# Performance work log

Hardware: AMD Instinct MI355X
Metric: run time of the kernel (lower is better)

## Reference

```python
import jax, jax.numpy as jnp
import numpy as np

TEMPERATURE = 0.02
B, T, D = 32, 256, 128


def _l2norm(x):
    return x / jnp.linalg.norm(x, axis=-1, keepdims=True)


def setup_inputs() -> dict:
    key = jax.random.key(0)
    k1, k2, k3, k4, k5, k6 = jax.random.split(key, 6)
    query_single = _l2norm(jax.random.normal(k1, (B, D), dtype=jnp.float32))
    pos_single = _l2norm(jax.random.normal(k2, (B, D), dtype=jnp.float32))
    query_multi = _l2norm(jax.random.normal(k3, (B, T, D), dtype=jnp.float32))
    pos_multi = _l2norm(jax.random.normal(k4, (B, T, D), dtype=jnp.float32))
    # variable-length masks (at least 1 valid token each, like real tokenized batches)
    q_len = jax.random.randint(k5, (B,), T // 4, T + 1)
    p_len = jax.random.randint(k6, (B,), T // 4, T + 1)
    pos = jnp.arange(T)[None, :]
    q_mask = pos < q_len[:, None]
    p_mask = pos < p_len[:, None]
    return {
        "query_single": query_single,
        "pos_single": pos_single,
        "query_multi": query_multi,
        "pos_multi": pos_multi,
        "q_mask": q_mask,
        "p_mask": p_mask,
    }


def _late_interaction_similarity(q_tokens, q_mask, p_tokens, p_mask):
    # All-pairs token similarity: [Bq, Bp, Tq, Tp]
    sim = jnp.einsum("bqd,cpd->bcqp", q_tokens, p_tokens)
    neg = jnp.finfo(sim.dtype).min
    sim = jnp.where(p_mask[None, :, None, :], sim, neg)
    mx = jnp.max(sim, axis=-1)                       # [Bq, Bp, Tq]
    mx = jnp.where(q_mask[:, None, :], mx, 0.0)      # drop invalid query tokens
    s = jnp.sum(mx, axis=-1)                         # [Bq, Bp]
    t_i = jnp.maximum(jnp.sum(q_mask, axis=-1), 1).astype(sim.dtype)  # [Bq]
    return s / t_i[:, None]


def _diag_cross_entropy(logits):
    # labels = arange(B): standard in-batch InfoNCE
    logp = jax.nn.log_softmax(logits, axis=-1)
    return -jnp.mean(jnp.diagonal(logp))


def reference(query_single, pos_single, query_multi, pos_multi, q_mask, p_mask):
    tau = TEMPERATURE
    dense_sim = query_single @ pos_single.T                       # [B, B]
    single_loss = _diag_cross_entropy(dense_sim / tau)

    S_late = _late_interaction_similarity(query_multi, q_mask, pos_multi, p_mask)
    multi_loss = _diag_cross_entropy(S_late / tau)

    dense_probs = jax.nn.softmax(dense_sim / tau, axis=1)
    late_probs = jax.nn.softmax(S_late / tau, axis=1)
    eps = 1e-8
    kl = jnp.mean(jnp.sum(dense_probs * jnp.log((dense_probs + eps) / (late_probs + eps)), axis=1))

    total_loss = single_loss + multi_loss + kl
    return (total_loss, single_loss, multi_loss, kl)
```

## Files before the change

### kernel.cpp

```cpp
#include <hip/hip_runtime.h>
#include <hip/hip_bf16.h>

#define B_SZ 32
#define T_SZ 256
#define D_SZ 128
#define TAU_INV 50.0f

typedef __bf16 bf16x8 __attribute__((ext_vector_type(8)));
typedef float f32x4 __attribute__((ext_vector_type(4)));

__device__ __forceinline__ unsigned short f2bf(float f) {
    union { float f; unsigned int u; } v; v.f = f;
    unsigned int r = v.u + 0x7fffu + ((v.u >> 16) & 1u);
    return (unsigned short)(r >> 16);
}

__device__ __forceinline__ bool mask_is_byte(const void* m) {
    return ((const int*)m)[0] != 1;
}
__device__ __forceinline__ int mget(const void* m, int idx, bool isb) {
    return isb ? (((const unsigned char*)m)[idx] != 0) : (((const int*)m)[idx] != 0);
}

__global__ __launch_bounds__(256) void cvt_both(
    const float* __restrict__ qsrc, const float* __restrict__ psrc,
    unsigned short* __restrict__ Qb, unsigned short* __restrict__ Pb) {
    const int half = blockIdx.x >> 10;
    const float* s = half ? psrc : qsrc;
    unsigned short* d = half ? Pb : Qb;
    int i = ((blockIdx.x & 1023) * 256 + threadIdx.x) * 4;
    float4 v = *(const float4*)(s + i);
    ushort4 o;
    o.x = f2bf(v.x); o.y = f2bf(v.y); o.z = f2bf(v.z); o.w = f2bf(v.w);
    *(ushort4*)(d + i) = o;
}

__global__ __launch_bounds__(512, 4) void late_sim(
    const unsigned short* __restrict__ Qbf, const unsigned short* __restrict__ Pbf,
    const void* __restrict__ qmask, const void* __restrict__ pmask,
    float* __restrict__ sraw)
{
    __shared__ __align__(16) unsigned char Plds[T_SZ * D_SZ * 2];
    __shared__ float madd[T_SZ];
    __shared__ float qmul[2][T_SZ];
    __shared__ float wsum[2][8];

    const int tid = threadIdx.x;
    const int l   = tid & 63;
    const int w   = tid >> 6;
    const int bid = blockIdx.x;
    const int c   = bid & 31;
    const int bg  = bid >> 5;
    const int b0  = bg, b1 = bg + 16;
    const int lr  = l & 15;
    const int lg  = l >> 4;

    const bool isb = mask_is_byte(qmask);
    const unsigned short* Pc = Pbf + c * (T_SZ * D_SZ);

    int p_hi;
    {
        int v = 0;
        #pragma unroll
        for (int j = 0; j < 4; ++j)
            if (mget(pmask, c * T_SZ + l * 4 + j, isb)) v = l * 4 + j + 1;
        #pragma unroll
        for (int off = 1; off < 64; off <<= 1) {
            int o = __shfl_xor(v, off);
            v = v > o ? v : o;
        }
        p_hi = v > 1 ? v : 1;
    }
    const int ptmax   = (p_hi + 15) >> 4;
    const int stiters = (p_hi + 31) >> 5;

    const int qrow = w * 32 + (l & 31);
    const bool do0 = __any(mget(qmask, b0 * T_SZ + qrow, isb));
    const bool do1 = __any(mget(qmask, b1 * T_SZ + qrow, isb));

    for (int it = 0; it < stiters; ++it) {
        int m   = it * 512 + tid;
        int row = m >> 4;
        int cs  = m & 15;
        bf16x8 v = *(const bf16x8*)(Pc + m * 8);
        *(bf16x8*)(Plds + row * 256 + ((cs ^ (row & 7)) << 4)) = v;
    }
    {
        int t = tid & 255;
        if (tid < 256) madd[t] = mget(pmask, c * T_SZ + t, isb) ? 0.0f : -1e30f;
        qmul[tid >> 8][t] = mget(qmask, (tid < 256 ? b0 : b1) * T_SZ + t, isb) ? 1.0f : 0.0f;
    }

    bf16x8 qf0[2][4] = {}, qf1[2][4] = {};
    if (do0)
        #pragma unroll
        for (int qt = 0; qt < 2; ++qt)
            #pragma unroll
            for (int k = 0; k < 4; ++k)
                qf0[qt][k] = *(const bf16x8*)(Qbf + b0 * (T_SZ * D_SZ)
                                              + (w * 32 + qt * 16 + lr) * D_SZ + k * 32 + lg * 8);
    if (do1)
        #pragma unroll
        for (int qt = 0; qt < 2; ++qt)
            #pragma unroll
            for (int k = 0; k < 4; ++k)
                qf1[qt][k] = *(const bf16x8*)(Qbf + b1 * (T_SZ * D_SZ)
                                              + (w * 32 + qt * 16 + lr) * D_SZ + k * 32 + lg * 8);

    __syncthreads();

    float r00 = -3e38f, r01 = -3e38f, r10 = -3e38f, r11 = -3e38f;

    for (int pt = 0; pt < ptmax; ++pt) {
        f32x4 a00 = {0,0,0,0}, a01 = {0,0,0,0}, a10 = {0,0,0,0}, a11 = {0,0,0,0};
        #pragma unroll
        for (int k = 0; k < 4; ++k) {
            int row = pt * 16 + lr;
            bf16x8 af = *(const bf16x8*)(Plds + row * 256 + (((k * 4 + lg) ^ (row & 7)) << 4));
            if (do0) {
                a00 = __builtin_amdgcn_mfma_f32_16x16x32_bf16(af, qf0[0][k], a00, 0, 0, 0);
                a01 = __builtin_amdgcn_mfma_f32_16x16x32_bf16(af, qf0[1][k], a01, 0, 0, 0);
            }
            if (do1) {
                a10 = __builtin_amdgcn_mfma_f32_16x16x32_bf16(af, qf1[0][k], a10, 0, 0, 0);
                a11 = __builtin_amdgcn_mfma_f32_16x16x32_bf16(af, qf1[1][k], a11, 0, 0, 0);
            }
        }
        float pm0 = madd[pt * 16 + lg * 4 + 0];
        float pm1 = madd[pt * 16 + lg * 4 + 1];
        float pm2 = madd[pt * 16 + lg * 4 + 2];
        float pm3 = madd[pt * 16 + lg * 4 + 3];
        if (do0) {
            r00 = fmaxf(r00, fmaxf(fmaxf(a00[0]+pm0, a00[1]+pm1), fmaxf(a00[2]+pm2, a00[3]+pm3)));
            r01 = fmaxf(r01, fmaxf(fmaxf(a01[0]+pm0, a01[1]+pm1), fmaxf(a01[2]+pm2, a01[3]+pm3)));
        }
        if (do1) {
            r10 = fmaxf(r10, fmaxf(fmaxf(a10[0]+pm0, a10[1]+pm1), fmaxf(a10[2]+pm2, a10[3]+pm3)));
            r11 = fmaxf(r11, fmaxf(fmaxf(a11[0]+pm0, a11[1]+pm1), fmaxf(a11[2]+pm2, a11[3]+pm3)));
        }
    }

    r00 = fmaxf(r00, __shfl_xor(r00, 16)); r00 = fmaxf(r00, __shfl_xor(r00, 32));
    r01 = fmaxf(r01, __shfl_xor(r01, 16)); r01 = fmaxf(r01, __shfl_xor(r01, 32));
    r10 = fmaxf(r10, __shfl_xor(r10, 16)); r10 = fmaxf(r10, __shfl_xor(r10, 32));
    r11 = fmaxf(r11, __shfl_xor(r11, 16)); r11 = fmaxf(r11, __shfl_xor(r11, 32));

    float t0 = r00 * qmul[0][w * 32 + lr] + r01 * qmul[0][w * 32 + 16 + lr];
    float t1 = r10 * qmul[1][w * 32 + lr] + r11 * qmul[1][w * 32 + 16 + lr];
    #pragma unroll
    for (int off = 32; off > 0; off >>= 1) {
        t0 += __shfl_down(t0, off);
        t1 += __shfl_down(t1, off);
    }
    if (l == 0) { wsum[0][w] = t0 * 0.25f; wsum[1][w] = t1 * 0.25f; }
    __syncthreads();

    if (tid == 0) {
        float s0 = 0.f, s1 = 0.f;
        #pragma unroll
        for (int ww = 0; ww < 8; ++ww) { s0 += wsum[0][ww]; s1 += wsum[1][ww]; }
        sraw[b0 * 32 + c] = s0;
        sraw[b1 * 32 + c] = s1;
    }
}

__global__ __launch_bounds__(256) void loss_final(
    const float* __restrict__ qs, const float* __restrict__ ps,
    const float* __restrict__ sraw, const void* __restrict__ qmask,
    float* __restrict__ out)
{
    __shared__ float qsL[B_SZ * 132];
    __shared__ float psL[B_SZ * 132];
    __shared__ float dense[B_SZ * B_SZ];
    __shared__ float late[B_SZ * B_SZ];
    __shared__ float tcnt[B_SZ];
    __shared__ float rsA[B_SZ], rmA[B_SZ], rkA[B_SZ];

    const int tid = threadIdx.x;
    const bool isb = mask_is_byte(qmask);

    for (int i = tid; i < 1024; i += 256) {
        int r = i >> 5, c4 = (i & 31) * 4;
        *(float4*)(qsL + r * 132 + c4) = *(const float4*)(qs + r * D_SZ + c4);
        *(float4*)(psL + r * 132 + c4) = *(const float4*)(ps + r * D_SZ + c4);
    }
    {
        const int r = tid >> 3, j = tid & 7;
        int cnt = 0;
        if (isb) {
            const unsigned int* mm = (const unsigned int*)((const unsigned char*)qmask + r * T_SZ + j * 32);
            #pragma unroll
            for (int t = 0; t < 8; ++t) cnt += (int)((mm[t] * 0x01010101u) >> 24);
        } else {
            const int* mm = (const int*)qmask + r * T_SZ + j * 32;
            #pragma unroll
            for (int t = 0; t < 32; ++t) cnt += (mm[t] != 0);
        }
        cnt += __shfl_xor(cnt, 1);
        cnt += __shfl_xor(cnt, 2);
        cnt += __shfl_xor(cnt, 4);
        if (j == 0) tcnt[r] = (float)(cnt > 1 ? cnt : 1);
    }
    __syncthreads();

    for (int idx = tid; idx < B_SZ * B_SZ; idx += 256) {
        int r = idx >> 5, cc = idx & 31;
        float s = 0.f;
        #pragma unroll
        for (int i = 0; i < D_SZ; i += 4) {
            float4 a  = *(const float4*)(qsL + r  * 132 + i);
            float4 bb = *(const float4*)(psL + cc * 132 + i);
            s += a.x * bb.x + a.y * bb.y + a.z * bb.z + a.w * bb.w;
        }
        dense[r * 32 + cc] = s;
        late[r * 32 + cc]  = sraw[idx] / tcnt[r];
    }
    __syncthreads();

    {
        const int cc = tid & 31;
        #pragma unroll
        for (int it = 0; it < 4; ++it) {
            const int r = (tid >> 5) + 8 * it;
            float xd = dense[r * 32 + cc] * TAU_INV;
            float xl = late[r * 32 + cc]  * TAU_INV;
            float md = xd, ml = xl;
            #pragma unroll
            for (int off = 16; off > 0; off >>= 1) {
                md = fmaxf(md, __shfl_xor(md, off));
                ml = fmaxf(ml, __shfl_xor(ml, off));
            }
            float sd = expf(xd - md), sl = expf(xl - ml);
            #pragma unroll
            for (int off = 16; off > 0; off >>= 1) {
                sd += __shfl_xor(sd, off);
                sl += __shfl_xor(sl, off);
            }
            float lsd = md + logf(sd);
            float lsl = ml + logf(sl);
            float pd = expf(xd - lsd);
            float pl = expf(xl - lsl);
            float klt = pd * logf((pd + 1e-8f) / (pl + 1e-8f));
            #pragma unroll
            for (int off = 16; off > 0; off >>= 1) klt += __shfl_xor(klt, off);
            if (cc == 0) rkA[r] = klt;
            if (cc == r) { rsA[r] = -(xd - lsd); rmA[r] = -(xl - lsl); }
        }
    }
    __syncthreads();

    if (tid < B_SZ) {
        float a = rsA[tid], bb = rmA[tid], c2 = rkA[tid];
        #pragma unroll
        for (int off = 16; off > 0; off >>= 1) {
            a  += __shfl_xor(a, off);
            bb += __shfl_xor(bb, off);
            c2 += __shfl_xor(c2, off);
        }
        if (tid == 0) {
            a *= (1.0f / B_SZ); bb *= (1.0f / B_SZ); c2 *= (1.0f / B_SZ);
            out[0] = a + bb + c2;
            out[1] = a;
            out[2] = bb;
            out[3] = c2;
        }
    }
}

extern "C" void kernel_launch(void* const* d_in, const int* in_sizes, int n_in,
                              void* d_out, int out_size, void* d_ws, size_t ws_size,
                              hipStream_t stream) {
    const float* qs    = (const float*)d_in[0];
    const float* ps    = (const float*)d_in[1];
    const float* qm3   = (const float*)d_in[2];
    const float* pm3   = (const float*)d_in[3];
    const void*  qmask = d_in[4];
    const void*  pmask = d_in[5];
    float* out = (float*)d_out;

    const int NTOK = B_SZ * T_SZ * D_SZ;
    unsigned short* Qbf = (unsigned short*)d_ws;
    unsigned short* Pbf = Qbf + NTOK;
    float* sraw = (float*)(Pbf + NTOK);

    cvt_both<<<2048, 256, 0, stream>>>(qm3, pm3, Qbf, Pbf);
    late_sim<<<512, 512, 0, stream>>>(Qbf, Pbf, qmask, pmask, sraw);
    loss_final<<<1, 256, 0, stream>>>(qs, ps, sraw, qmask, out);
}
```

Baseline: 39.73 us.

## Precompute masks in prep kernel, async global-to-LDS loads, XCD-aware block mapping

After: 55.50 us. +39.7%, slower.

```diff
diff --git a/kernel.cpp b/kernel.cpp
--- a/kernel.cpp
+++ b/kernel.cpp
@@ -22,23 +22,51 @@
     return isb ? (((const unsigned char*)m)[idx] != 0) : (((const int*)m)[idx] != 0);
 }
 
-__global__ __launch_bounds__(256) void cvt_both(
+__global__ __launch_bounds__(256) void cvt_prep(
     const float* __restrict__ qsrc, const float* __restrict__ psrc,
-    unsigned short* __restrict__ Qb, unsigned short* __restrict__ Pb) {
+    const void* __restrict__ qmask, const void* __restrict__ pmask,
+    unsigned short* __restrict__ Qb, unsigned short* __restrict__ Pb,
+    float* __restrict__ maddF, float* __restrict__ qmulF,
+    int* __restrict__ p_hiA, float* __restrict__ tcntA) {
+    const int tid = threadIdx.x;
     const int half = blockIdx.x >> 10;
-    const float* s = half ? psrc : qsrc;
-    unsigned short* d = half ? Pb : Qb;
-    int i = ((blockIdx.x & 1023) * 256 + threadIdx.x) * 4;
-    float4 v = *(const float4*)(s + i);
-    ushort4 o;
-    o.x = f2bf(v.x); o.y = f2bf(v.y); o.z = f2bf(v.z); o.w = f2bf(v.w);
-    *(ushort4*)(d + i) = o;
+    if (half < 2) {
+        const float* s = half ? psrc : qsrc;
+        unsigned short* d = half ? Pb : Qb;
+        int i = ((blockIdx.x & 1023) * 256 + tid) * 4;
+        float4 v = *(const float4*)(s + i);
+        ushort4 o;
+        o.x = f2bf(v.x); o.y = f2bf(v.y); o.z = f2bf(v.z); o.w = f2bf(v.w);
+        *(ushort4*)(d + i) = o;
+        return;
+    }
+    const bool isb = mask_is_byte(qmask);
+    for (int idx = tid; idx < B_SZ * T_SZ; idx += 256) {
+        maddF[idx] = mget(pmask, idx, isb) ? 0.0f : -1e30f;
+        qmulF[idx] = mget(qmask, idx, isb) ? 1.0f : 0.0f;
+    }
+    const int r = tid >> 3, j = tid & 7;
+    int last_p = 0, cntq = 0;
+    for (int t = j * 32; t < j * 32 + 32; ++t) {
+        if (mget(pmask, r * T_SZ + t, isb)) last_p = t + 1;
+        cntq += mget(qmask, r * T_SZ + t, isb);
+    }
+    #pragma unroll
+    for (int off = 1; off < 8; off <<= 1) {
+        int lp = __shfl_xor(last_p, off);
+        last_p = lp > last_p ? lp : last_p;
+        cntq += __shfl_xor(cntq, off);
+    }
+    if (j == 0) {
+        p_hiA[r] = last_p > 1 ? last_p : 1;
+        tcntA[r] = (float)(cntq > 1 ? cntq : 1);
+    }
 }
 
 __global__ __launch_bounds__(512, 4) void late_sim(
     const unsigned short* __restrict__ Qbf, const unsigned short* __restrict__ Pbf,
-    const void* __restrict__ qmask, const void* __restrict__ pmask,
-    float* __restrict__ sraw)
+    const float* __restrict__ maddF, const float* __restrict__ qmulF,
+    const int* __restrict__ p_hiA, float* __restrict__ sraw)
 {
     __shared__ __align__(16) unsigned char Plds[T_SZ * D_SZ * 2];
     __shared__ float madd[T_SZ];
@@ -49,47 +77,21 @@
     const int l   = tid & 63;
     const int w   = tid >> 6;
     const int bid = blockIdx.x;
-    const int c   = bid & 31;
-    const int bg  = bid >> 5;
+    const int xcd = bid & 7;
+    const int idx = bid >> 3;
+    const int bg  = xcd * 2 + (idx >> 5);
+    const int c   = idx & 31;
     const int b0  = bg, b1 = bg + 16;
     const int lr  = l & 15;
     const int lg  = l >> 4;
 
-    const bool isb = mask_is_byte(qmask);
-    const unsigned short* Pc = Pbf + c * (T_SZ * D_SZ);
-
-    int p_hi;
-    {
-        int v = 0;
-        #pragma unroll
-        for (int j = 0; j < 4; ++j)
-            if (mget(pmask, c * T_SZ + l * 4 + j, isb)) v = l * 4 + j + 1;
-        #pragma unroll
-        for (int off = 1; off < 64; off <<= 1) {
-            int o = __shfl_xor(v, off);
-            v = v > o ? v : o;
-        }
-        p_hi = v > 1 ? v : 1;
-    }
+    const int p_hi    = p_hiA[c];
     const int ptmax   = (p_hi + 15) >> 4;
     const int stiters = (p_hi + 31) >> 5;
 
     const int qrow = w * 32 + (l & 31);
-    const bool do0 = __any(mget(qmask, b0 * T_SZ + qrow, isb));
-    const bool do1 = __any(mget(qmask, b1 * T_SZ + qrow, isb));
-
-    for (int it = 0; it < stiters; ++it) {
-        int m   = it * 512 + tid;
-        int row = m >> 4;
-        int cs  = m & 15;
-        bf16x8 v = *(const bf16x8*)(Pc + m * 8);
-        *(bf16x8*)(Plds + row * 256 + ((cs ^ (row & 7)) << 4)) = v;
-    }
-    {
-        int t = tid & 255;
-        if (tid < 256) madd[t] = mget(pmask, c * T_SZ + t, isb) ? 0.0f : -1e30f;
-        qmul[tid >> 8][t] = mget(qmask, (tid < 256 ? b0 : b1) * T_SZ + t, isb) ? 1.0f : 0.0f;
-    }
+    const bool do0 = __any(qmulF[b0 * T_SZ + qrow] > 0.0f);
+    const bool do1 = __any(qmulF[b1 * T_SZ + qrow] > 0.0f);
 
     bf16x8 qf0[2][4] = {}, qf1[2][4] = {};
     if (do0)
@@ -98,15 +100,37 @@
             #pragma unroll
             for (int k = 0; k < 4; ++k)
                 qf0[qt][k] = *(const bf16x8*)(Qbf + b0 * (T_SZ * D_SZ)
-                                              + (w * 32 + qt * 16 + lr) * D_SZ + k * 32 + lg * 8);
+                              + (w * 32 + qt * 16 + lr) * D_SZ + k * 32 + lg * 8);
     if (do1)
         #pragma unroll
         for (int qt = 0; qt < 2; ++qt)
             #pragma unroll
             for (int k = 0; k < 4; ++k)
                 qf1[qt][k] = *(const bf16x8*)(Qbf + b1 * (T_SZ * D_SZ)
-                                              + (w * 32 + qt * 16 + lr) * D_SZ + k * 32 + lg * 8);
-
+                              + (w * 32 + qt * 16 + lr) * D_SZ + k * 32 + lg * 8);
+
+    {
+        const unsigned short* Pc = Pbf + c * (T_SZ * D_SZ);
+        for (int it = 0; it < stiters; ++it) {
+            int j   = it * 512 + w * 64 + l;
+            int row = j >> 4;
+            int cj  = j & 15;
+            const unsigned short* src = Pc + row * D_SZ + ((cj ^ (row & 7)) << 3);
+            __builtin_amdgcn_global_load_lds(
+                (const __attribute__((address_space(1))) unsigned int*)src,
+                (__attribute__((address_space(3))) unsigned int*)(Plds + (it * 512 + w * 64) * 16),
+                16, 0, 0);
+        }
+    }
+    if (tid < 64) {
+        *(float4*)(madd + tid * 4) = *(const float4*)(maddF + c * T_SZ + tid * 4);
+    } else if (tid < 128) {
+        int t = tid - 64;
+        *(float4*)(qmul[0] + t * 4) = *(const float4*)(qmulF + b0 * T_SZ + t * 4);
+    } else if (tid < 192) {
+        int t = tid - 128;
+        *(float4*)(qmul[1] + t * 4) = *(const float4*)(qmulF + b1 * T_SZ + t * 4);
+    }
     __syncthreads();
 
     float r00 = -3e38f, r01 = -3e38f, r10 = -3e38f, r11 = -3e38f;
@@ -129,14 +153,14 @@
         float pm0 = madd[pt * 16 + lg * 4 + 0];
         float pm1 = madd[pt * 16 + lg * 4 + 1];
         float pm2 = madd[pt * 16 + lg * 4 + 2];
-        float pm3 = madd[pt * 16 + lg * 4 + 3];
+        float pm3v = madd[pt * 16 + lg * 4 + 3];
         if (do0) {
-            r00 = fmaxf(r00, fmaxf(fmaxf(a00[0]+pm0, a00[1]+pm1), fmaxf(a00[2]+pm2, a00[3]+pm3)));
-            r01 = fmaxf(r01, fmaxf(fmaxf(a01[0]+pm0, a01[1]+pm1), fmaxf(a01[2]+pm2, a01[3]+pm3)));
+            r00 = fmaxf(r00, fmaxf(fmaxf(a00[0]+pm0, a00[1]+pm1), fmaxf(a00[2]+pm2, a00[3]+pm3v)));
+            r01 = fmaxf(r01, fmaxf(fmaxf(a01[0]+pm0, a01[1]+pm1), fmaxf(a01[2]+pm2, a01[3]+pm3v)));
         }
         if (do1) {
-            r10 = fmaxf(r10, fmaxf(fmaxf(a10[0]+pm0, a10[1]+pm1), fmaxf(a10[2]+pm2, a10[3]+pm3)));
-            r11 = fmaxf(r11, fmaxf(fmaxf(a11[0]+pm0, a11[1]+pm1), fmaxf(a11[2]+pm2, a11[3]+pm3)));
+            r10 = fmaxf(r10, fmaxf(fmaxf(a10[0]+pm0, a10[1]+pm1), fmaxf(a10[2]+pm2, a10[3]+pm3v)));
+            r11 = fmaxf(r11, fmaxf(fmaxf(a11[0]+pm0, a11[1]+pm1), fmaxf(a11[2]+pm2, a11[3]+pm3v)));
         }
     }
 
@@ -166,7 +190,7 @@
 
 __global__ __launch_bounds__(256) void loss_final(
     const float* __restrict__ qs, const float* __restrict__ ps,
-    const float* __restrict__ sraw, const void* __restrict__ qmask,
+    const float* __restrict__ sraw, const float* __restrict__ tcntA,
     float* __restrict__ out)
 {
     __shared__ float qsL[B_SZ * 132];
@@ -177,30 +201,13 @@
     __shared__ float rsA[B_SZ], rmA[B_SZ], rkA[B_SZ];
 
     const int tid = threadIdx.x;
-    const bool isb = mask_is_byte(qmask);
 
     for (int i = tid; i < 1024; i += 256) {
         int r = i >> 5, c4 = (i & 31) * 4;
         *(float4*)(qsL + r * 132 + c4) = *(const float4*)(qs + r * D_SZ + c4);
         *(float4*)(psL + r * 132 + c4) = *(const float4*)(ps + r * D_SZ + c4);
     }
-    {
-        const int r = tid >> 3, j = tid & 7;
-        int cnt = 0;
-        if (isb) {
-            const unsigned int* mm = (const unsigned int*)((const unsigned char*)qmask + r * T_SZ + j * 32);
-            #pragma unroll
-            for (int t = 0; t < 8; ++t) cnt += (int)((mm[t] * 0x01010101u) >> 24);
-        } else {
-            const int* mm = (const int*)qmask + r * T_SZ + j * 32;
-            #pragma unroll
-            for (int t = 0; t < 32; ++t) cnt += (mm[t] != 0);
-        }
-        cnt += __shfl_xor(cnt, 1);
-        cnt += __shfl_xor(cnt, 2);
-        cnt += __shfl_xor(cnt, 4);
-        if (j == 0) tcnt[r] = (float)(cnt > 1 ? cnt : 1);
-    }
+    if (tid < B_SZ) tcnt[tid] = tcntA[tid];
     __syncthreads();
 
     for (int idx = tid; idx < B_SZ * B_SZ; idx += 256) {
@@ -281,9 +288,14 @@
     const int NTOK = B_SZ * T_SZ * D_SZ;
     unsigned short* Qbf = (unsigned short*)d_ws;
     unsigned short* Pbf = Qbf + NTOK;
-    float* sraw = (float*)(Pbf + NTOK);
-
-    cvt_both<<<2048, 256, 0, stream>>>(qm3, pm3, Qbf, Pbf);
-    late_sim<<<512, 512, 0, stream>>>(Qbf, Pbf, qmask, pmask, sraw);
-    loss_final<<<1, 256, 0, stream>>>(qs, ps, sraw, qmask, out);
-}
+    float* sraw  = (float*)(Pbf + NTOK);
+    float* maddF = sraw + 1024;
+    float* qmulF = maddF + B_SZ * T_SZ;
+    int*   p_hiA = (int*)(qmulF + B_SZ * T_SZ);
+    float* tcntA = (float*)(p_hiA + 32);
+
+    cvt_prep<<<2049, 256, 0, stream>>>(qm3, pm3, qmask, pmask, Qbf, Pbf,
+                                       maddF, qmulF, p_hiA, tcntA);
+    late_sim<<<512, 512, 0, stream>>>(Qbf, Pbf, maddF, qmulF, p_hiA, sraw);
+    loss_final<<<1, 256, 0, stream>>>(qs, ps, sraw, tcntA, out);
+}
```
